# Kernel optimization log

Measured on AMD Instinct MI355X. Metric: run time of the kernel, lower is better.

The kernel has to match this reference:

```python
import jax, jax.numpy as jnp
import numpy as np

EPS = 1e-5

def headwise_linear(x, w):
    # x: [B,S,D], w: [NH, DH_out, DH_in] block-diagonal linear per head
    B, S, D = x.shape
    NH, O, DH = w.shape
    xh = x.reshape(B, S, NH, DH)
    return jnp.einsum('bshd,hod->bsho', xh, w).reshape(B, S, NH * O)

def setup_inputs() -> dict:
    key = jax.random.key(0)
    ks = jax.random.split(key, 10)
    B, S, D, NH, K = 8, 4096, 768, 4, 4
    DH = D // NH
    small = (2.0 / (5.0 * D)) ** 0.5  # small_init scale
    return {
        'x': jax.random.normal(ks[0], (B, S, D), jnp.float32),
        'conv_w': jax.random.normal(ks[1], (D, 1, K), jnp.float32) * (1.0 / K ** 0.5),
        'conv_b': jnp.zeros((D,), jnp.float32),
        'w_f': jax.random.normal(ks[2], (NH, DH, DH), jnp.float32) * small,
        'w_i': jax.random.normal(ks[3], (NH, DH, DH), jnp.float32) * small,
        'w_z': jax.random.normal(ks[4], (NH, DH, DH), jnp.float32) * small,
        'w_o': jax.random.normal(ks[5], (NH, DH, DH), jnp.float32) * small,
        'r_kernel': jax.random.normal(ks[6], (NH, DH, 4, DH), jnp.float32) * (1.0 / DH ** 0.5),
        'r_bias': jnp.zeros((4, NH, DH), jnp.float32),
        'gn_weight': jnp.ones((D,), jnp.float32),
    }

def reference(x, conv_w, conv_b, w_f, w_i, w_z, w_o, r_kernel, r_bias, gn_weight):
    B, S, D = x.shape
    NH, DH = r_kernel.shape[0], r_kernel.shape[1]
    K = conv_w.shape[-1]
    # --- causal depthwise conv1d + SiLU ---
    xt = jnp.transpose(x, (0, 2, 1))  # [B,D,S]
    xc = jax.lax.conv_general_dilated(xt, conv_w, (1,), [(K - 1, 0)],
                                      feature_group_count=D)
    x_conv = jax.nn.silu(jnp.transpose(xc + conv_b[None, :, None], (0, 2, 1)))
    # --- headwise gate projections (note: original code feeds fgate->i, igate->f) ---
    gi = headwise_linear(x_conv, w_f)
    gf = headwise_linear(x_conv, w_i)
    gz = headwise_linear(x, w_z)
    go = headwise_linear(x, w_o)
    Wx = jnp.stack([gi, gf, gz, go], axis=2).reshape(B, S, 4, NH, DH)
    Wx = jnp.transpose(Wx, (1, 0, 2, 3, 4))  # [S,B,4,NH,DH]
    # --- sLSTM recurrent scan with exponential gating + stabilizer m ---
    def step(carry, wx_t):
        y, c, n, m = carry  # each [B,NH,DH]
        Ry = jnp.einsum('bhd,hdge->bghe', y, r_kernel)  # [B,4,NH,DH]
        raw = wx_t + Ry + r_bias[None]
        iraw, fraw, zraw, oraw = raw[:, 0], raw[:, 1], raw[:, 2], raw[:, 3]
        logfplusm = m + jax.nn.log_sigmoid(fraw)
        mnew = jnp.maximum(iraw, logfplusm)
        igate = jnp.exp(iraw - mnew)
        fgate = jnp.exp(logfplusm - mnew)
        cnew = fgate * c + igate * jnp.tanh(zraw)
        nnew = fgate * n + igate
        ynew = jax.nn.sigmoid(oraw) * cnew / nnew
        return (ynew, cnew, nnew, mnew), ynew
    init = tuple(jnp.zeros((B, NH, DH), x.dtype) for _ in range(4))
    _, ys = jax.lax.scan(step, init, Wx)  # [S,B,NH,DH]
    y = jnp.transpose(ys, (1, 2, 0, 3))  # [B,NH,S,DH]
    # --- multi-head layer norm (group norm with NH groups over DH) ---
    mean = y.mean(-1, keepdims=True)
    var = y.var(-1, keepdims=True)
    yn = (y - mean) * jax.lax.rsqrt(var + EPS)
    yn = yn * gn_weight.reshape(1, NH, 1, DH)
    return jnp.transpose(yn, (0, 2, 1, 3)).reshape(B, S, NH * DH)
```

## Files before the change

kernel.cpp:

```cpp
#include <hip/hip_runtime.h>
#include <hip/hip_bf16.h>
#include <math.h>

#define B_ 8
#define S_ 4096
#define D_ 768
#define NH_ 4
#define DH_ 192
#define NTOT_ 768

typedef __attribute__((ext_vector_type(8))) short short8;
typedef __attribute__((ext_vector_type(4))) float floatx4;
typedef _Float16 f16;
typedef __attribute__((ext_vector_type(2))) _Float16 h2;

__device__ __forceinline__ short f2bs(float f) {
  union { float f; unsigned u; } v; v.f = f;
  unsigned r = v.u + 0x7FFFu + ((v.u >> 16) & 1u);
  return (short)(r >> 16);
}
__device__ __forceinline__ float bs2f(unsigned short s) {
  union { unsigned u; float f; } v; v.u = ((unsigned)s) << 16;
  return v.f;
}

#if __has_builtin(__builtin_amdgcn_fdot2)
__device__ __forceinline__ float FDOT2(h2 a, h2 b, float c) {
  return __builtin_amdgcn_fdot2(a, b, c, false);
}
#else
__device__ __forceinline__ float FDOT2(h2 a, h2 b, float c) {
  return c + (float)a.x * (float)b.x + (float)a.y * (float)b.y;
}
#endif

template<int CTRL>
__device__ __forceinline__ float qbcast(float x) {
  return __int_as_float(__builtin_amdgcn_mov_dpp(__float_as_int(x), CTRL, 0xf, 0xf, true));
}

__global__ __launch_bounds__(256) void wconv_kernel(
    const float* __restrict__ wf, const float* __restrict__ wi,
    const float* __restrict__ wz, const float* __restrict__ wo,
    short* __restrict__ Wbf)
{
  int idx = blockIdx.x * 256 + threadIdx.x;
  int hg = idx / (DH_ * DH_);
  int r  = idx % (DH_ * DH_);
  int h = hg >> 2, g = hg & 3;
  const float* W = (g == 0) ? wf : (g == 1) ? wi : (g == 2) ? wz : wo;
  Wbf[idx] = f2bs(W[(size_t)h * DH_ * DH_ + r]);
}

__global__ __launch_bounds__(256) void conv_silu_kernel(
    const float* __restrict__ x, const float* __restrict__ cw, const float* __restrict__ cb,
    short* __restrict__ xb, short* __restrict__ xcb)
{
  const int b  = blockIdx.x / (S_ / 64);
  const int s0 = (blockIdx.x % (S_ / 64)) * 64;
  const int tid = threadIdx.x;
  float wv[3][4], bias[3], win[3][3];
  for (int j = 0; j < 3; ++j) {
    int d = tid + j * 256;
    for (int k = 0; k < 4; ++k) wv[j][k] = cw[d * 4 + k];
    bias[j] = cb[d];
    for (int p = 0; p < 3; ++p) {
      int s = s0 - 3 + p;
      win[j][p] = (s >= 0) ? x[((size_t)b * S_ + s) * D_ + d] : 0.f;
    }
  }
  for (int i = 0; i < 64; ++i) {
    size_t base = ((size_t)b * S_ + (s0 + i)) * D_;
    for (int j = 0; j < 3; ++j) {
      int d = tid + j * 256;
      float xc = x[base + d];
      float a = bias[j] + win[j][0] * wv[j][0] + win[j][1] * wv[j][1]
                        + win[j][2] * wv[j][2] + xc * wv[j][3];
      float sv = a / (1.f + __expf(-a));
      xb[base + d]  = f2bs(xc);
      xcb[base + d] = f2bs(sv);
      win[j][0] = win[j][1]; win[j][1] = win[j][2]; win[j][2] = xc;
    }
  }
}

__global__ __launch_bounds__(256) void proj_kernel(
    const short* __restrict__ xb, const short* __restrict__ xcb,
    const short* __restrict__ Wbf, short* __restrict__ P)
{
  const int hg = blockIdx.y;
  const int h = hg >> 2, g = hg & 3;
  const short* A  = (g < 2) ? xcb : xb;
  const short* Wb = Wbf + (size_t)hg * (DH_ * DH_);
  const int tid = threadIdx.x, w = tid >> 6, l = tid & 63;
  const int l15 = l & 15, lg = l >> 4;
  const int R0 = blockIdx.x * 256 + w * 64;

  for (int mp = 0; mp < 2; ++mp) {
    const int rb0 = R0 + mp * 32;
    floatx4 acc[2][12];
    for (int u = 0; u < 2; ++u)
      for (int nt = 0; nt < 12; ++nt) acc[u][nt] = (floatx4){0.f, 0.f, 0.f, 0.f};
    const short* Ar = A + (size_t)(rb0 + l15) * D_ + h * DH_ + lg * 8;
    const short* Bp = Wb + l15 * DH_ + lg * 8;
    for (int kk = 0; kk < 6; ++kk) {
      short8 a0 = *(const short8*)(Ar + kk * 32);
      short8 a1 = *(const short8*)(Ar + (size_t)16 * D_ + kk * 32);
      for (int nt = 0; nt < 12; ++nt) {
        short8 bf = *(const short8*)(Bp + nt * 16 * DH_ + kk * 32);
        acc[0][nt] = __builtin_amdgcn_mfma_f32_16x16x32_bf16(a0, bf, acc[0][nt], 0, 0, 0);
        acc[1][nt] = __builtin_amdgcn_mfma_f32_16x16x32_bf16(a1, bf, acc[1][nt], 0, 0, 0);
      }
    }
    for (int u = 0; u < 2; ++u) {
      for (int q = 0; q < 4; ++q) {
        int row = rb0 + u * 16 + lg * 4 + q;
        int s = row & (S_ - 1);
        int bb = row >> 12;
        size_t ob = (((size_t)h * B_ + bb) * S_ + s) * NTOT_ + g * DH_ + l15;
        for (int nt = 0; nt < 12; ++nt) P[ob + nt * 16] = f2bs(acc[u][nt][q]);
      }
    }
  }
}

__global__ __launch_bounds__(768) void scan_kernel(
    short* P_, const float* __restrict__ rk, const float* __restrict__ rb)
{
  const int bid = blockIdx.x;
  const int h = bid >> 3;
  const int t0 = threadIdx.x;
  const int e = t0 >> 2, g = t0 & 3;

  __shared__ __align__(16) f16 y_lds[2][DH_];

  h2 Rr[96];
  {
    const float* Rc = rk + (size_t)h * (DH_ * NTOT_) + g * DH_ + e;
#pragma unroll
    for (int j = 0; j < 96; ++j) {
      float v0 = Rc[(size_t)(2 * j) * NTOT_];
      float v1 = Rc[(size_t)(2 * j + 1) * NTOT_];
      Rr[j] = (h2){(f16)v0, (f16)v1};
    }
  }
  const float biasv = rb[(g * NH_ + h) * DH_ + e];
  if (t0 < DH_) y_lds[0][t0] = (f16)0.f;

  float c = 0.f, nrm = 0.f, m = 0.f;
  short* Pc = P_ + (size_t)bid * S_ * NTOT_;
  const int addr = g * DH_ + e;
  float wxc = bs2f((unsigned short)Pc[addr]);
  __syncthreads();

#pragma unroll 1
  for (int t = 0; t < S_; ++t) {
    unsigned short wxn = 0;
    if (t + 1 < S_) wxn = (unsigned short)Pc[(size_t)(t + 1) * NTOT_ + addr];

    const int cur = t & 1, nxt = cur ^ 1;
    const f16* yb = &y_lds[cur][0];
    float a0 = 0.f, a1 = 0.f, a2 = 0.f, a3 = 0.f;
#pragma unroll
    for (int j = 0; j < 96; j += 4) {
      h2 y0 = *(const h2*)(yb + 2 * j);
      h2 y1 = *(const h2*)(yb + 2 * j + 2);
      h2 y2 = *(const h2*)(yb + 2 * j + 4);
      h2 y3 = *(const h2*)(yb + 2 * j + 6);
      a0 = FDOT2(Rr[j],     y0, a0);
      a1 = FDOT2(Rr[j + 1], y1, a1);
      a2 = FDOT2(Rr[j + 2], y2, a2);
      a3 = FDOT2(Rr[j + 3], y3, a3);
    }
    float raw = wxc + ((a0 + a1) + (a2 + a3)) + biasv;

    float ir  = qbcast<0x00>(raw);
    float fr  = qbcast<0x55>(raw);
    float zr  = qbcast<0xAA>(raw);
    float orr = qbcast<0xFF>(raw);

    float lsf = fminf(fr, 0.f) - __logf(1.f + __expf(-fabsf(fr)));
    float lfm = m + lsf;
    float mnew = fmaxf(ir, lfm);
    float ig = __expf(ir - mnew);
    float fg = __expf(lfm - mnew);
    float e2z = __expf(2.f * zr);
    float tz = 1.f - 2.f / (e2z + 1.f);
    c   = fg * c + ig * tz;
    nrm = fg * nrm + ig;
    m = mnew;
    float sg = 1.f / (1.f + __expf(-orr));
    float y = sg * c / nrm;

    f16 yh = (f16)y;
    if (g == 0) {
      y_lds[nxt][e] = yh;
      union { f16 h; short s; } uv; uv.h = yh;
      Pc[(size_t)t * NTOT_ + e] = uv.s;
    }
    wxc = bs2f(wxn);
    __syncthreads();
  }
}

__global__ __launch_bounds__(256) void gnorm_kernel(
    const short* __restrict__ yws, const float* __restrict__ gnw,
    float* __restrict__ out)
{
  const int row = blockIdx.x * 4 + (threadIdx.x >> 6);
  const int l = threadIdx.x & 63;
  const int h = row >> 15;
  const int b = (row >> 12) & 7;
  const int s = row & (S_ - 1);
  const short* yr = yws + (size_t)row * NTOT_;
  float v[3];
  float su = 0.f, sq = 0.f;
#pragma unroll
  for (int j = 0; j < 3; ++j) {
    unsigned short u = (unsigned short)yr[l + j * 64];
    union { unsigned short u; f16 h; } cv; cv.u = u;
    v[j] = (float)cv.h;
    su += v[j]; sq += v[j] * v[j];
  }
  for (int off = 32; off; off >>= 1) {
    su += __shfl_xor(su, off);
    sq += __shfl_xor(sq, off);
  }
  float mean = su * (1.f / DH_);
  float var = sq * (1.f / DH_) - mean * mean;
  float rs = rsqrtf(var + 1e-5f);
  float* orow = out + ((size_t)b * S_ + s) * D_ + h * DH_;
#pragma unroll
  for (int j = 0; j < 3; ++j)
    orow[l + j * 64] = (v[j] - mean) * rs * gnw[h * DH_ + l + j * 64];
}

extern "C" void kernel_launch(void* const* d_in, const int* in_sizes, int n_in,
                              void* d_out, int out_size, void* d_ws, size_t ws_size,
                              hipStream_t stream) {
  const float* x   = (const float*)d_in[0];
  const float* cw  = (const float*)d_in[1];
  const float* cb  = (const float*)d_in[2];
  const float* wf  = (const float*)d_in[3];
  const float* wi  = (const float*)d_in[4];
  const float* wz  = (const float*)d_in[5];
  const float* wo  = (const float*)d_in[6];
  const float* rk  = (const float*)d_in[7];
  const float* rb  = (const float*)d_in[8];
  const float* gnw = (const float*)d_in[9];
  float* out = (float*)d_out;

  short* P   = (short*)d_ws;
  short* Wbf = (short*)((char*)d_ws + (size_t)201326592);
  short* xb  = (short*)d_out;
  short* xcb = (short*)((char*)d_out + (size_t)50331648);

  wconv_kernel<<<dim3(2304), 256, 0, stream>>>(wf, wi, wz, wo, Wbf);
  conv_silu_kernel<<<dim3(512), 256, 0, stream>>>(x, cw, cb, xb, xcb);
  proj_kernel<<<dim3(128, 16), 256, 0, stream>>>(xb, xcb, Wbf, P);
  scan_kernel<<<dim3(32), 768, 0, stream>>>(P, rk, rb);
  gnorm_kernel<<<dim3(32768), 256, 0, stream>>>(P, gnw, out);
}
```

Before: 5.831 ms.

## Split scan recurrence over K-quarters with DPP reduction and interleaved gate layout

The scan kernel used to give each of the four lanes in a quad one gate over the full 192-long dot product. Now each lane covers a quarter of the K dimension for all four gates and the partial sums are combined with DPP quad-permute adds. Each lane now reads 48 y values from LDS as wide h8 loads instead of all 192, which cuts LDS traffic per step. To match, the projection kernel writes the four gate pre-activations interleaved, so each thread fetches its four gate inputs with one 8-byte load. The cost is eight extra DPP adds on the serial critical path and every lane computing the same gate math redundantly.

```diff
diff --git a/kernel.cpp b/kernel.cpp
--- a/kernel.cpp
+++ b/kernel.cpp
@@ -11,8 +11,10 @@
 
 typedef __attribute__((ext_vector_type(8))) short short8;
 typedef __attribute__((ext_vector_type(4))) float floatx4;
+typedef __attribute__((ext_vector_type(4))) short short4v;
 typedef _Float16 f16;
 typedef __attribute__((ext_vector_type(2))) _Float16 h2;
+typedef __attribute__((ext_vector_type(8))) _Float16 h8;
 
 __device__ __forceinline__ short f2bs(float f) {
   union { float f; unsigned u; } v; v.f = f;
@@ -35,7 +37,7 @@
 #endif
 
 template<int CTRL>
-__device__ __forceinline__ float qbcast(float x) {
+__device__ __forceinline__ float qperm(float x) {
   return __int_as_float(__builtin_amdgcn_mov_dpp(__float_as_int(x), CTRL, 0xf, 0xf, true));
 }
 
@@ -117,8 +119,8 @@
         int row = rb0 + u * 16 + lg * 4 + q;
         int s = row & (S_ - 1);
         int bb = row >> 12;
-        size_t ob = (((size_t)h * B_ + bb) * S_ + s) * NTOT_ + g * DH_ + l15;
-        for (int nt = 0; nt < 12; ++nt) P[ob + nt * 16] = f2bs(acc[u][nt][q]);
+        size_t ob = (((size_t)h * B_ + bb) * S_ + s) * NTOT_ + l15 * 4 + g;
+        for (int nt = 0; nt < 12; ++nt) P[ob + nt * 64] = f2bs(acc[u][nt][q]);
       }
     }
   }
@@ -130,54 +132,64 @@
   const int bid = blockIdx.x;
   const int h = bid >> 3;
   const int t0 = threadIdx.x;
-  const int e = t0 >> 2, g = t0 & 3;
+  const int e = t0 >> 2, q = t0 & 3;
 
   __shared__ __align__(16) f16 y_lds[2][DH_];
 
-  h2 Rr[96];
+  h2 Rr[4][24];
   {
-    const float* Rc = rk + (size_t)h * (DH_ * NTOT_) + g * DH_ + e;
-#pragma unroll
-    for (int j = 0; j < 96; ++j) {
-      float v0 = Rc[(size_t)(2 * j) * NTOT_];
-      float v1 = Rc[(size_t)(2 * j + 1) * NTOT_];
-      Rr[j] = (h2){(f16)v0, (f16)v1};
-    }
-  }
-  const float biasv = rb[(g * NH_ + h) * DH_ + e];
+    const float* Rh = rk + (size_t)h * (DH_ * NTOT_);
+#pragma unroll
+    for (int j = 0; j < 24; ++j) {
+      const int k0 = 48 * q + 2 * j;
+#pragma unroll
+      for (int g = 0; g < 4; ++g) {
+        float v0 = Rh[((size_t)k0 * 4 + g) * DH_ + e];
+        float v1 = Rh[((size_t)(k0 + 1) * 4 + g) * DH_ + e];
+        Rr[g][j] = (h2){(f16)v0, (f16)v1};
+      }
+    }
+  }
+  float biasv[4];
+#pragma unroll
+  for (int g = 0; g < 4; ++g) biasv[g] = rb[(g * NH_ + h) * DH_ + e];
+
   if (t0 < DH_) y_lds[0][t0] = (f16)0.f;
 
   float c = 0.f, nrm = 0.f, m = 0.f;
   short* Pc = P_ + (size_t)bid * S_ * NTOT_;
-  const int addr = g * DH_ + e;
-  float wxc = bs2f((unsigned short)Pc[addr]);
+  short4v wxc = *(const short4v*)(Pc + e * 4);
   __syncthreads();
 
 #pragma unroll 1
   for (int t = 0; t < S_; ++t) {
-    unsigned short wxn = 0;
-    if (t + 1 < S_) wxn = (unsigned short)Pc[(size_t)(t + 1) * NTOT_ + addr];
-
-    const int cur = t & 1, nxt = cur ^ 1;
-    const f16* yb = &y_lds[cur][0];
+    short4v wxn = {};
+    if (t + 1 < S_) wxn = *(const short4v*)(Pc + (size_t)(t + 1) * NTOT_ + e * 4);
+
+    const f16* yb = &y_lds[t & 1][q * 48];
     float a0 = 0.f, a1 = 0.f, a2 = 0.f, a3 = 0.f;
 #pragma unroll
-    for (int j = 0; j < 96; j += 4) {
-      h2 y0 = *(const h2*)(yb + 2 * j);
-      h2 y1 = *(const h2*)(yb + 2 * j + 2);
-      h2 y2 = *(const h2*)(yb + 2 * j + 4);
-      h2 y3 = *(const h2*)(yb + 2 * j + 6);
-      a0 = FDOT2(Rr[j],     y0, a0);
-      a1 = FDOT2(Rr[j + 1], y1, a1);
-      a2 = FDOT2(Rr[j + 2], y2, a2);
-      a3 = FDOT2(Rr[j + 3], y3, a3);
-    }
-    float raw = wxc + ((a0 + a1) + (a2 + a3)) + biasv;
-
-    float ir  = qbcast<0x00>(raw);
-    float fr  = qbcast<0x55>(raw);
-    float zr  = qbcast<0xAA>(raw);
-    float orr = qbcast<0xFF>(raw);
+    for (int i = 0; i < 6; ++i) {
+      h8 ch = ((const h8*)yb)[i];
+#pragma unroll
+      for (int u = 0; u < 4; ++u) {
+        h2 yp = (h2){ch[2 * u], ch[2 * u + 1]};
+        const int j = i * 4 + u;
+        a0 = FDOT2(Rr[0][j], yp, a0);
+        a1 = FDOT2(Rr[1][j], yp, a1);
+        a2 = FDOT2(Rr[2][j], yp, a2);
+        a3 = FDOT2(Rr[3][j], yp, a3);
+      }
+    }
+    a0 += qperm<0xB1>(a0);  a0 += qperm<0x4E>(a0);
+    a1 += qperm<0xB1>(a1);  a1 += qperm<0x4E>(a1);
+    a2 += qperm<0xB1>(a2);  a2 += qperm<0x4E>(a2);
+    a3 += qperm<0xB1>(a3);  a3 += qperm<0x4E>(a3);
+
+    float ir  = bs2f((unsigned short)wxc[0]) + a0 + biasv[0];
+    float fr  = bs2f((unsigned short)wxc[1]) + a1 + biasv[1];
+    float zr  = bs2f((unsigned short)wxc[2]) + a2 + biasv[2];
+    float orr = bs2f((unsigned short)wxc[3]) + a3 + biasv[3];
 
     float lsf = fminf(fr, 0.f) - __logf(1.f + __expf(-fabsf(fr)));
     float lfm = m + lsf;
@@ -193,12 +205,12 @@
     float y = sg * c / nrm;
 
     f16 yh = (f16)y;
-    if (g == 0) {
-      y_lds[nxt][e] = yh;
-      union { f16 h; short s; } uv; uv.h = yh;
-      Pc[(size_t)t * NTOT_ + e] = uv.s;
-    }
-    wxc = bs2f(wxn);
+    if (q == 0) {
+      y_lds[(t & 1) ^ 1][e] = yh;
+      union { f16 hh; short ss; } uv; uv.hh = yh;
+      Pc[(size_t)t * NTOT_ + e] = uv.ss;
+    }
+    wxc = wxn;
     __syncthreads();
   }
 }
```

Result: faster. 5.580 ms (-4.3%).
